# Kernel tuning notes

Measured on AMD Instinct MI355X. Metric: run time of the kernel, lower is better.

## Reference

```python
import jax, jax.numpy as jnp
import numpy as np

N = 20000      # nodes
E = 320000     # edges
D = 512        # width
L = 4          # layers
VOCAB = 256
MAX_POS = 256
EPS = 1e-5


def setup_inputs() -> dict:
    key = jax.random.key(0)
    ks = jax.random.split(key, 12)
    tokens = jax.random.randint(ks[0], (N,), 0, VOCAB)
    pos = jax.random.randint(ks[1], (N,), 0, MAX_POS)
    edge_index = jax.random.randint(ks[2], (2, E), 0, N)
    vocab_emb = jax.random.normal(ks[3], (VOCAB, D), jnp.float32) * 0.05
    pos_emb = jax.random.normal(ks[4], (MAX_POS, D), jnp.float32) * 0.05
    bn_gamma = jnp.ones((L, D), jnp.float32)
    bn_beta = jnp.zeros((L, D), jnp.float32)
    bn_mean = jax.random.normal(ks[5], (L, D), jnp.float32) * 0.1
    bn_var = jax.random.uniform(ks[6], (L, D), jnp.float32, 0.5, 1.5)
    W_rel = jax.random.normal(ks[7], (L, D, D), jnp.float32) * (1.0 / np.sqrt(D))
    b_rel = jnp.zeros((L, D), jnp.float32)
    W_root = jax.random.normal(ks[8], (L, D, D), jnp.float32) * (1.0 / np.sqrt(D))
    return {
        "tokens": tokens, "pos": pos, "edge_index": edge_index,
        "vocab_emb": vocab_emb, "pos_emb": pos_emb,
        "bn_gamma": bn_gamma, "bn_beta": bn_beta,
        "bn_mean": bn_mean, "bn_var": bn_var,
        "W_rel": W_rel, "b_rel": b_rel, "W_root": W_root,
    }


def reference(tokens, pos, edge_index, vocab_emb, pos_emb,
              bn_gamma, bn_beta, bn_mean, bn_var, W_rel, b_rel, W_root):
    src, dst = edge_index[0], edge_index[1]
    # in-degree for mean aggregation (clamped to 1 like PyG mean aggr)
    deg = jax.ops.segment_sum(jnp.ones((E,), jnp.float32), dst, num_segments=N)
    deg = jnp.maximum(deg, 1.0)[:, None]                     # [N,1]

    x = vocab_emb[tokens] + pos_emb[pos]                     # [N,D]
    for l in range(L):
        # BatchNorm1d, eval mode with running stats
        inv = bn_gamma[l] * jax.lax.rsqrt(bn_var[l] + EPS)
        x = (x - bn_mean[l]) * inv + bn_beta[l]
        # GraphConv: W_root x_i + W_rel * mean_{j->i} x_j + b
        agg = jax.ops.segment_sum(x[src], dst, num_segments=N) / deg
        x = agg @ W_rel[l].T + b_rel[l] + x @ W_root[l].T
        x = jax.nn.relu(x)
    return x
```

## Files before the change

kernel.cpp:

```cpp
#include <hip/hip_runtime.h>
#include <cstdint>

#define EPS 1e-5f

typedef __attribute__((ext_vector_type(8))) short bf16x8;
typedef __attribute__((ext_vector_type(4))) float f32x4;

__device__ __forceinline__ unsigned short f2bf(float x) {
    uint32_t u = __float_as_uint(x);
    u += 0x7fffu + ((u >> 16) & 1u);
    return (unsigned short)(u >> 16);
}
__device__ __forceinline__ uint32_t pack2(float lo, float hi) {
    return (uint32_t)f2bf(lo) | ((uint32_t)f2bf(hi) << 16);
}
__device__ __forceinline__ float bflo(uint32_t p) { return __uint_as_float(p << 16); }
__device__ __forceinline__ float bfhi(uint32_t p) { return __uint_as_float(p & 0xffff0000u); }

__device__ __forceinline__ void async_ld16(const void* g, const void* l) {
    __builtin_amdgcn_global_load_lds(
        (const __attribute__((address_space(1))) uint32_t*)(uintptr_t)g,
        (__attribute__((address_space(3))) uint32_t*)(uint32_t)(uintptr_t)l,
        16, 0, 0);
}

__global__ __launch_bounds__(256) void zero_kernel(int* __restrict__ p, int n) {
    int i = blockIdx.x * 256 + threadIdx.x;
    if (i < n) p[i] = 0;
}

__global__ __launch_bounds__(256) void count_kernel(const int* __restrict__ ei,
                                                    int* __restrict__ deg, int E) {
    int e = blockIdx.x * 256 + threadIdx.x;
    if (e < E) atomicAdd(&deg[ei[E + e]], 1);
}

__global__ __launch_bounds__(1024) void scan_kernel(const int* __restrict__ deg,
                                                    int* __restrict__ offsets,
                                                    int* __restrict__ cursor,
                                                    float* __restrict__ deginv, int N) {
    __shared__ int part[1024];
    const int t = threadIdx.x;
    const int CH = (N + 1023) >> 10;
    const int base = t * CH;
    int s = 0;
    for (int j = 0; j < CH; ++j) {
        int idx = base + j;
        if (idx < N) s += deg[idx];
    }
    part[t] = s;
    __syncthreads();
    for (int off = 1; off < 1024; off <<= 1) {
        int add = (t >= off) ? part[t - off] : 0;
        __syncthreads();
        part[t] += add;
        __syncthreads();
    }
    int run = (t == 0) ? 0 : part[t - 1];
    for (int j = 0; j < CH; ++j) {
        int idx = base + j;
        if (idx < N) {
            offsets[idx] = run;
            cursor[idx]  = run;
            int dgi = deg[idx];
            deginv[idx] = 1.0f / (float)(dgi > 0 ? dgi : 1);
            run += dgi;
        }
    }
    if (t == 1023) offsets[N] = run;
}

__global__ __launch_bounds__(256) void fill_kernel(const int* __restrict__ ei,
                                                   int* __restrict__ cursor,
                                                   int* __restrict__ csr, int E) {
    int e = blockIdx.x * 256 + threadIdx.x;
    if (e < E) {
        int dd = ei[E + e];
        int slot = atomicAdd(&cursor[dd], 1);
        csr[slot] = ei[e];
    }
}

__global__ __launch_bounds__(256) void embed_bn_kernel(const int* __restrict__ tok,
                                                       const int* __restrict__ pos,
                                                       const float* __restrict__ vemb,
                                                       const float* __restrict__ pemb,
                                                       const float* __restrict__ gamma,
                                                       const float* __restrict__ beta,
                                                       const float* __restrict__ mean,
                                                       const float* __restrict__ var,
                                                       uint32_t* __restrict__ Acat, int N) {
    const int idx = blockIdx.x * 256 + threadIdx.x;
    if (idx >= N * 128) return;
    const int row = idx >> 7;
    const int c = (idx & 127) * 4;
    const int tk = tok[row];
    const int ps = pos[row];
    const float4 a = *(const float4*)&vemb[(size_t)tk * 512 + c];
    const float4 b = *(const float4*)&pemb[(size_t)ps * 512 + c];
    const float4 g = *(const float4*)&gamma[c];
    const float4 be = *(const float4*)&beta[c];
    const float4 mn = *(const float4*)&mean[c];
    const float4 vr = *(const float4*)&var[c];
    const float y0 = (a.x + b.x - mn.x) * (g.x * rsqrtf(vr.x + EPS)) + be.x;
    const float y1 = (a.y + b.y - mn.y) * (g.y * rsqrtf(vr.y + EPS)) + be.y;
    const float y2 = (a.z + b.z - mn.z) * (g.z * rsqrtf(vr.z + EPS)) + be.z;
    const float y3 = (a.w + b.w - mn.w) * (g.w * rsqrtf(vr.w + EPS)) + be.w;
    uint2 o;
    o.x = pack2(y0, y1);
    o.y = pack2(y2, y3);
    *(uint2*)&Acat[(size_t)row * 512 + (c >> 1)] = o;
}

__global__ __launch_bounds__(256) void castW_kernel(const float* __restrict__ Wroot,
                                                    const float* __restrict__ Wrel,
                                                    uint32_t* __restrict__ Wcat) {
    const int p = blockIdx.x * 256 + threadIdx.x;
    const int o  = p >> 9;
    const int dp = p & 511;
    float2 v;
    if (dp < 256) v = *(const float2*)&Wroot[(size_t)o * 512 + dp * 2];
    else          v = *(const float2*)&Wrel[(size_t)o * 512 + (dp - 256) * 2];
    Wcat[(size_t)o * 512 + dp] = pack2(v.x, v.y);
}

__global__ __launch_bounds__(256) void aggregate_kernel(uint32_t* __restrict__ Acat,
                                                        const int* __restrict__ offsets,
                                                        const int* __restrict__ csr,
                                                        const float* __restrict__ deginv,
                                                        int N) {
    const int node = blockIdx.x * 4 + (threadIdx.x >> 6);
    if (node >= N) return;
    const int lane = threadIdx.x & 63;
    const int col = lane * 4;
    const int beg = offsets[node];
    const int end = offsets[node + 1];
    float s[8] = {0.f, 0.f, 0.f, 0.f, 0.f, 0.f, 0.f, 0.f};
    int e = beg;
    for (; e + 4 <= end; e += 4) {
        const int i0 = csr[e];
        const int i1 = csr[e + 1];
        const int i2 = csr[e + 2];
        const int i3 = csr[e + 3];
        const uint4 p0 = *(const uint4*)&Acat[(size_t)i0 * 512 + col];
        const uint4 p1 = *(const uint4*)&Acat[(size_t)i1 * 512 + col];
        const uint4 p2 = *(const uint4*)&Acat[(size_t)i2 * 512 + col];
        const uint4 p3 = *(const uint4*)&Acat[(size_t)i3 * 512 + col];
        s[0] += bflo(p0.x) + bflo(p1.x) + bflo(p2.x) + bflo(p3.x);
        s[1] += bfhi(p0.x) + bfhi(p1.x) + bfhi(p2.x) + bfhi(p3.x);
        s[2] += bflo(p0.y) + bflo(p1.y) + bflo(p2.y) + bflo(p3.y);
        s[3] += bfhi(p0.y) + bfhi(p1.y) + bfhi(p2.y) + bfhi(p3.y);
        s[4] += bflo(p0.z) + bflo(p1.z) + bflo(p2.z) + bflo(p3.z);
        s[5] += bfhi(p0.z) + bfhi(p1.z) + bfhi(p2.z) + bfhi(p3.z);
        s[6] += bflo(p0.w) + bflo(p1.w) + bflo(p2.w) + bflo(p3.w);
        s[7] += bfhi(p0.w) + bfhi(p1.w) + bfhi(p2.w) + bfhi(p3.w);
    }
    for (; e < end; ++e) {
        const int i0 = csr[e];
        const uint4 p0 = *(const uint4*)&Acat[(size_t)i0 * 512 + col];
        s[0] += bflo(p0.x); s[1] += bfhi(p0.x);
        s[2] += bflo(p0.y); s[3] += bfhi(p0.y);
        s[4] += bflo(p0.z); s[5] += bfhi(p0.z);
        s[6] += bflo(p0.w); s[7] += bfhi(p0.w);
    }
    const float inv = deginv[node];
    uint4 o;
    o.x = pack2(s[0] * inv, s[1] * inv);
    o.y = pack2(s[2] * inv, s[3] * inv);
    o.z = pack2(s[4] * inv, s[5] * inv);
    o.w = pack2(s[6] * inv, s[7] * inv);
    *(uint4*)&Acat[(size_t)node * 512 + 256 + col] = o;
}

__global__ __launch_bounds__(256) void gemm_bt_bias_relu(const unsigned short* __restrict__ A,
                                                         const unsigned short* __restrict__ B,
                                                         const float* __restrict__ bias,
                                                         const float* __restrict__ gamma,
                                                         const float* __restrict__ beta,
                                                         const float* __restrict__ mean,
                                                         const float* __restrict__ var,
                                                         int last,
                                                         float* __restrict__ C,
                                                         unsigned short* __restrict__ Abn,
                                                         int M) {
    __shared__ __align__(16) unsigned short As[128 * 32];
    __shared__ __align__(16) unsigned short Bs[128 * 32];

    const int t    = threadIdx.x;
    const int lane = t & 63;
    const int wave = t >> 6;
    const int wm = (wave >> 1) * 64;
    const int wn = (wave & 1) * 64;
    const int bm = blockIdx.y;
    const int bn = blockIdx.x;

    const int r  = t >> 2;
    const int kc = t & 3;
    int ar0 = bm * 128 + r;      if (ar0 >= M) ar0 = M - 1;
    int ar1 = bm * 128 + r + 64; if (ar1 >= M) ar1 = M - 1;
    const int br0 = bn * 128 + r;
    const int br1 = br0 + 64;

    const unsigned short* ga0 = A + (size_t)ar0 * 1024 + kc * 8;
    const unsigned short* ga1 = A + (size_t)ar1 * 1024 + kc * 8;
    const unsigned short* gb0 = B + (size_t)br0 * 1024 + kc * 8;
    const unsigned short* gb1 = B + (size_t)br1 * 1024 + kc * 8;

    unsigned short* la0 = &As[r * 32 + kc * 8];
    unsigned short* la1 = &As[(r + 64) * 32 + kc * 8];
    unsigned short* lb0 = &Bs[r * 32 + kc * 8];
    unsigned short* lb1 = &Bs[(r + 64) * 32 + kc * 8];

    const f32x4 zero = {0.f, 0.f, 0.f, 0.f};
    f32x4 acc[4][4];
#pragma unroll
    for (int i = 0; i < 4; ++i)
#pragma unroll
        for (int j = 0; j < 4; ++j) acc[i][j] = zero;

    const int lm = lane & 15;
    const int q  = lane >> 4;

    for (int k0 = 0; k0 < 1024; k0 += 32) {
        async_ld16(ga0 + k0, la0);
        async_ld16(ga1 + k0, la1);
        async_ld16(gb0 + k0, lb0);
        async_ld16(gb1 + k0, lb1);
        __syncthreads();

        bf16x8 afr[4], bfr[4];
#pragma unroll
        for (int mt = 0; mt < 4; ++mt)
            afr[mt] = *(const bf16x8*)&As[(wm + mt * 16 + lm) * 32 + q * 8];
#pragma unroll
        for (int nt = 0; nt < 4; ++nt)
            bfr[nt] = *(const bf16x8*)&Bs[(wn + nt * 16 + lm) * 32 + q * 8];
#pragma unroll
        for (int mt = 0; mt < 4; ++mt)
#pragma unroll
            for (int nt = 0; nt < 4; ++nt)
                acc[mt][nt] = __builtin_amdgcn_mfma_f32_16x16x32_bf16(afr[mt], bfr[nt],
                                                                     acc[mt][nt], 0, 0, 0);
        __syncthreads();
    }

#pragma unroll
    for (int nt = 0; nt < 4; ++nt) {
        const int col = bn * 128 + wn + nt * 16 + lm;
        const float bv = bias[col];
        float bn_inv = 0.f, bn_mb = 0.f;
        if (!last) {
            bn_inv = gamma[col] * rsqrtf(var[col] + EPS);
            bn_mb  = mean[col];
        }
        const float bn_beta = last ? 0.f : beta[col];
#pragma unroll
        for (int mt = 0; mt < 4; ++mt) {
            const int row0 = bm * 128 + wm + mt * 16 + q * 4;
#pragma unroll
            for (int i = 0; i < 4; ++i) {
                const int row = row0 + i;
                if (row < M) {
                    float v = acc[mt][nt][i] + bv;
                    v = v > 0.f ? v : 0.f;
                    if (last) {
                        C[(size_t)row * 512 + col] = v;
                    } else {
                        const float y = (v - bn_mb) * bn_inv + bn_beta;
                        Abn[(size_t)row * 1024 + col] = f2bf(y);
                    }
                }
            }
        }
    }
}

extern "C" void kernel_launch(void* const* d_in, const int* in_sizes, int n_in,
                              void* d_out, int out_size, void* d_ws, size_t ws_size,
                              hipStream_t stream) {
    const int*   tokens = (const int*)d_in[0];
    const int*   posi   = (const int*)d_in[1];
    const int*   ei     = (const int*)d_in[2];
    const float* vemb   = (const float*)d_in[3];
    const float* pemb   = (const float*)d_in[4];
    const float* gamma  = (const float*)d_in[5];
    const float* beta   = (const float*)d_in[6];
    const float* mean   = (const float*)d_in[7];
    const float* var    = (const float*)d_in[8];
    const float* Wrel   = (const float*)d_in[9];
    const float* brel   = (const float*)d_in[10];
    const float* Wroot  = (const float*)d_in[11];

    const int N = in_sizes[0];
    const int E = in_sizes[2] / 2;
    float* out = (float*)d_out;

    char* w = (char*)d_ws;
    int*      deg     = (int*)(w);
    int*      offsets = (int*)(w + 80000);
    int*      cursor  = (int*)(w + 160016);
    float*    deginv  = (float*)(w + 240032);
    int*      csr     = (int*)(w + 320048);
    uint32_t* Acat    = (uint32_t*)(w + 1600064);
    uint32_t* Wcat    = (uint32_t*)(w + 42560064);

    zero_kernel<<<(N + 255) / 256, 256, 0, stream>>>(deg, N);
    count_kernel<<<(E + 255) / 256, 256, 0, stream>>>(ei, deg, E);
    scan_kernel<<<1, 1024, 0, stream>>>(deg, offsets, cursor, deginv, N);
    fill_kernel<<<(E + 255) / 256, 256, 0, stream>>>(ei, cursor, csr, E);

    embed_bn_kernel<<<(N * 128 + 255) / 256, 256, 0, stream>>>(
        tokens, posi, vemb, pemb, gamma, beta, mean, var, Acat, N);

    for (int l = 0; l < 4; ++l) {
        const int last = (l == 3);
        castW_kernel<<<1024, 256, 0, stream>>>(Wroot + (size_t)l * 262144,
                                               Wrel + (size_t)l * 262144, Wcat);
        aggregate_kernel<<<(N + 3) / 4, 256, 0, stream>>>(Acat, offsets, csr, deginv, N);
        gemm_bt_bias_relu<<<dim3(4, (N + 127) / 128), 256, 0, stream>>>(
            (const unsigned short*)Acat, (const unsigned short*)Wcat, brel + l * 512,
            gamma + (l + 1) * 512, beta + (l + 1) * 512,
            mean + (l + 1) * 512, var + (l + 1) * 512,
            last, out, (unsigned short*)Acat, N);
    }
}
```

Baseline: 563.4 us.

## Replace GEMM with triple-buffered 256x128 tile kernel using swizzled LDS and XCD mapping

Replaces the single-buffered 128x128 GEMM with a 512-thread, 256x128-tile kernel. It uses a three-stage async global-to-LDS pipeline over K=64 slices with explicit vmcnt waits, XOR-swizzled LDS layout to avoid bank conflicts, and s_setprio around MFMA bursts. Block IDs are remapped so each XCD works on a contiguous band of row tiles, which is meant to improve L2 reuse of A. It uses 144 KB of dynamic LDS per block, which limits occupancy, and it relies on hand-counted waitcnt values.

```diff
diff --git a/kernel.cpp b/kernel.cpp
--- a/kernel.cpp
+++ b/kernel.cpp
@@ -172,44 +172,65 @@
     *(uint4*)&Acat[(size_t)node * 512 + 256 + col] = o;
 }
 
-__global__ __launch_bounds__(256) void gemm_bt_bias_relu(const unsigned short* __restrict__ A,
-                                                         const unsigned short* __restrict__ B,
-                                                         const float* __restrict__ bias,
-                                                         const float* __restrict__ gamma,
-                                                         const float* __restrict__ beta,
-                                                         const float* __restrict__ mean,
-                                                         const float* __restrict__ var,
-                                                         int last,
-                                                         float* __restrict__ C,
-                                                         unsigned short* __restrict__ Abn,
-                                                         int M) {
-    __shared__ __align__(16) unsigned short As[128 * 32];
-    __shared__ __align__(16) unsigned short Bs[128 * 32];
+__global__ __launch_bounds__(512, 2)
+void gemm_pipe(const unsigned short* __restrict__ A,
+               const unsigned short* __restrict__ B,
+               const float* __restrict__ bias,
+               const float* __restrict__ gamma,
+               const float* __restrict__ beta,
+               const float* __restrict__ mean,
+               const float* __restrict__ var,
+               int last,
+               float* __restrict__ C,
+               unsigned short* __restrict__ Abn,
+               int M, int mt, int rpx) {
+    extern __shared__ unsigned short lds[];
+
+    const int bid = blockIdx.x;
+    const int xcd = bid & 7;
+    const int slt = bid >> 3;
+    const int bm  = xcd * rpx + (slt >> 2);
+    const int bn  = slt & 3;
+    if (bm >= mt) return;
 
     const int t    = threadIdx.x;
     const int lane = t & 63;
-    const int wave = t >> 6;
-    const int wm = (wave >> 1) * 64;
-    const int wn = (wave & 1) * 64;
-    const int bm = blockIdx.y;
-    const int bn = blockIdx.x;
-
-    const int r  = t >> 2;
-    const int kc = t & 3;
-    int ar0 = bm * 128 + r;      if (ar0 >= M) ar0 = M - 1;
-    int ar1 = bm * 128 + r + 64; if (ar1 >= M) ar1 = M - 1;
-    const int br0 = bn * 128 + r;
-    const int br1 = br0 + 64;
-
-    const unsigned short* ga0 = A + (size_t)ar0 * 1024 + kc * 8;
-    const unsigned short* ga1 = A + (size_t)ar1 * 1024 + kc * 8;
-    const unsigned short* gb0 = B + (size_t)br0 * 1024 + kc * 8;
-    const unsigned short* gb1 = B + (size_t)br1 * 1024 + kc * 8;
-
-    unsigned short* la0 = &As[r * 32 + kc * 8];
-    unsigned short* la1 = &As[(r + 64) * 32 + kc * 8];
-    unsigned short* lb0 = &Bs[r * 32 + kc * 8];
-    unsigned short* lb1 = &Bs[(r + 64) * 32 + kc * 8];
+    const int wid  = t >> 6;
+    const int wr   = wid >> 1;
+    const int wc   = wid & 1;
+    const int lm   = lane & 15;
+    const int q    = lane >> 4;
+
+    const int tr = t >> 3;
+    const int sg = (t & 7) ^ (tr & 7);
+    int r0 = bm * 256 + tr;        if (r0 >= M) r0 = M - 1;
+    int r1 = bm * 256 + 64  + tr;  if (r1 >= M) r1 = M - 1;
+    int r2 = bm * 256 + 128 + tr;  if (r2 >= M) r2 = M - 1;
+    int r3 = bm * 256 + 192 + tr;  if (r3 >= M) r3 = M - 1;
+    const unsigned short* gA0 = A + (size_t)r0 * 1024 + sg * 8;
+    const unsigned short* gA1 = A + (size_t)r1 * 1024 + sg * 8;
+    const unsigned short* gA2 = A + (size_t)r2 * 1024 + sg * 8;
+    const unsigned short* gA3 = A + (size_t)r3 * 1024 + sg * 8;
+    const unsigned short* gB0 = B + (size_t)(bn * 128 + tr)      * 1024 + sg * 8;
+    const unsigned short* gB1 = B + (size_t)(bn * 128 + 64 + tr) * 1024 + sg * 8;
+    const int ldst = t * 8;
+
+#define STAGE_H0(KT, LP) do {                                          \
+        async_ld16(gA0 + (KT) * 64, (LP) + 0 * 4096 + ldst);           \
+        async_ld16(gA1 + (KT) * 64, (LP) + 1 * 4096 + ldst);           \
+        async_ld16(gA2 + (KT) * 64, (LP) + 2 * 4096 + ldst);           \
+    } while (0)
+#define STAGE_H1(KT, LP) do {                                          \
+        async_ld16(gA3 + (KT) * 64, (LP) + 3 * 4096 + ldst);           \
+        async_ld16(gB0 + (KT) * 64, (LP) + 16384 + 0 * 4096 + ldst);   \
+        async_ld16(gB1 + (KT) * 64, (LP) + 16384 + 1 * 4096 + ldst);   \
+    } while (0)
+
+    const int aB = (wr * 64 + lm) * 64;
+    const int bB = 16384 + (wc * 64 + lm) * 64;
+    const int sw = lm & 7;
+    const int k0 = ((0 + q) ^ sw) * 8;
+    const int k1 = ((4 + q) ^ sw) * 8;
 
     const f32x4 zero = {0.f, 0.f, 0.f, 0.f};
     f32x4 acc[4][4];
@@ -218,61 +239,74 @@
 #pragma unroll
         for (int j = 0; j < 4; ++j) acc[i][j] = zero;
 
-    const int lm = lane & 15;
-    const int q  = lane >> 4;
-
-    for (int k0 = 0; k0 < 1024; k0 += 32) {
-        async_ld16(ga0 + k0, la0);
-        async_ld16(ga1 + k0, la1);
-        async_ld16(gb0 + k0, lb0);
-        async_ld16(gb1 + k0, lb1);
-        __syncthreads();
-
-        bf16x8 afr[4], bfr[4];
-#pragma unroll
-        for (int mt = 0; mt < 4; ++mt)
-            afr[mt] = *(const bf16x8*)&As[(wm + mt * 16 + lm) * 32 + q * 8];
-#pragma unroll
-        for (int nt = 0; nt < 4; ++nt)
-            bfr[nt] = *(const bf16x8*)&Bs[(wn + nt * 16 + lm) * 32 + q * 8];
-#pragma unroll
-        for (int mt = 0; mt < 4; ++mt)
-#pragma unroll
-            for (int nt = 0; nt < 4; ++nt)
-                acc[mt][nt] = __builtin_amdgcn_mfma_f32_16x16x32_bf16(afr[mt], bfr[nt],
-                                                                     acc[mt][nt], 0, 0, 0);
-        __syncthreads();
-    }
-
-#pragma unroll
-    for (int nt = 0; nt < 4; ++nt) {
-        const int col = bn * 128 + wn + nt * 16 + lm;
-        const float bv = bias[col];
-        float bn_inv = 0.f, bn_mb = 0.f;
+#define MFMA_PHASE(KOFF) do {                                                   \
+        bf16x8 afr[4], bfr[4];                                                  \
+        _Pragma("unroll") for (int mf = 0; mf < 4; ++mf)                        \
+            afr[mf] = *(const bf16x8*)&Lb[aB + mf * 1024 + (KOFF)];             \
+        _Pragma("unroll") for (int nf = 0; nf < 4; ++nf)                        \
+            bfr[nf] = *(const bf16x8*)&Lb[bB + nf * 1024 + (KOFF)];             \
+        __builtin_amdgcn_s_setprio(1);                                          \
+        _Pragma("unroll") for (int mf = 0; mf < 4; ++mf)                        \
+            _Pragma("unroll") for (int nf = 0; nf < 4; ++nf)                    \
+                acc[mf][nf] = __builtin_amdgcn_mfma_f32_16x16x32_bf16(          \
+                    afr[mf], bfr[nf], acc[mf][nf], 0, 0, 0);                    \
+        __builtin_amdgcn_s_setprio(0);                                          \
+    } while (0)
+
+    {
+        unsigned short* L0 = lds;
+        STAGE_H0(0, L0); STAGE_H1(0, L0);
+        unsigned short* L1 = lds + 24576;
+        STAGE_H0(1, L1); STAGE_H1(1, L1);
+    }
+
+#pragma unroll
+    for (int kt = 0; kt < 16; ++kt) {
+        unsigned short* Lb = lds + (kt % 3) * 24576;
+        unsigned short* Ln = lds + ((kt + 2) % 3) * 24576;
+        if (kt < 15) asm volatile("s_waitcnt vmcnt(6)" ::: "memory");
+        else         asm volatile("s_waitcnt vmcnt(0)" ::: "memory");
+        __builtin_amdgcn_s_barrier();
+        __builtin_amdgcn_sched_barrier(0);
+
+        if (kt + 2 < 16) STAGE_H0(kt + 2, Ln);
+        MFMA_PHASE(k0);
+        if (kt + 2 < 16) STAGE_H1(kt + 2, Ln);
+        MFMA_PHASE(k1);
+    }
+
+#pragma unroll
+    for (int nf = 0; nf < 4; ++nf) {
+        const int col = bn * 128 + wc * 64 + nf * 16 + lm;
+        const float bsv = bias[col];
+        float bn_inv = 0.f, bn_mb = 0.f, bn_bt = 0.f;
         if (!last) {
             bn_inv = gamma[col] * rsqrtf(var[col] + EPS);
             bn_mb  = mean[col];
+            bn_bt  = beta[col];
         }
-        const float bn_beta = last ? 0.f : beta[col];
-#pragma unroll
-        for (int mt = 0; mt < 4; ++mt) {
-            const int row0 = bm * 128 + wm + mt * 16 + q * 4;
+#pragma unroll
+        for (int mf = 0; mf < 4; ++mf) {
+            const int row0 = bm * 256 + wr * 64 + mf * 16 + q * 4;
 #pragma unroll
             for (int i = 0; i < 4; ++i) {
                 const int row = row0 + i;
                 if (row < M) {
-                    float v = acc[mt][nt][i] + bv;
+                    float v = acc[mf][nf][i] + bsv;
                     v = v > 0.f ? v : 0.f;
                     if (last) {
                         C[(size_t)row * 512 + col] = v;
                     } else {
-                        const float y = (v - bn_mb) * bn_inv + bn_beta;
+                        const float y = (v - bn_mb) * bn_inv + bn_bt;
                         Abn[(size_t)row * 1024 + col] = f2bf(y);
                     }
                 }
             }
         }
     }
+#undef STAGE_H0
+#undef STAGE_H1
+#undef MFMA_PHASE
 }
 
 extern "C" void kernel_launch(void* const* d_in, const int* in_sizes, int n_in,
@@ -304,6 +338,13 @@
     uint32_t* Acat    = (uint32_t*)(w + 1600064);
     uint32_t* Wcat    = (uint32_t*)(w + 42560064);
 
+    static bool s_attr = false;
+    if (!s_attr) {
+        (void)hipFuncSetAttribute(reinterpret_cast<const void*>(gemm_pipe),
+                                  hipFuncAttributeMaxDynamicSharedMemorySize, 147456);
+        s_attr = true;
+    }
+
     zero_kernel<<<(N + 255) / 256, 256, 0, stream>>>(deg, N);
     count_kernel<<<(E + 255) / 256, 256, 0, stream>>>(ei, deg, E);
     scan_kernel<<<1, 1024, 0, stream>>>(deg, offsets, cursor, deginv, N);
@@ -311,16 +352,20 @@
 
     embed_bn_kernel<<<(N * 128 + 255) / 256, 256, 0, stream>>>(
         tokens, posi, vemb, pemb, gamma, beta, mean, var, Acat, N);
+
+    const int mt  = (N + 255) >> 8;
+    const int rpx = (mt + 7) >> 3;
+    const int gb  = 8 * rpx * 4;
 
     for (int l = 0; l < 4; ++l) {
         const int last = (l == 3);
         castW_kernel<<<1024, 256, 0, stream>>>(Wroot + (size_t)l * 262144,
                                                Wrel + (size_t)l * 262144, Wcat);
         aggregate_kernel<<<(N + 3) / 4, 256, 0, stream>>>(Acat, offsets, csr, deginv, N);
-        gemm_bt_bias_relu<<<dim3(4, (N + 127) / 128), 256, 0, stream>>>(
+        gemm_pipe<<<gb, 512, 147456, stream>>>(
             (const unsigned short*)Acat, (const unsigned short*)Wcat, brel + l * 512,
             gamma + (l + 1) * 512, beta + (l + 1) * 512,
             mean + (l + 1) * 512, var + (l + 1) * 512,
-            last, out, (unsigned short*)Acat, N);
-    }
-}
+            last, out, (unsigned short*)Acat, N, mt, rpx);
+    }
+}
```

Result: slower. 597.1 us (+6.0%).

## Widen GEMM K-step to 64, swizzle block order, batch weight casts

Applied to the files above, without the earlier changes.

The GEMM now loads two 32-wide K slices per iteration, which halves the number of barrier pairs and issues more MFMAs between syncs. Blocks move to a 1D grid whose index is remapped so that consecutive blocks are spread across eight row groups, with the four column tiles of a row block kept adjacent, to change cache/XCD locality. When the workspace is large enough, all four layers' weights are cast to bf16 in one kernel up front instead of once per layer. This doubles LDS use per block and relies on a workspace-size check to choose the path.

```diff
diff --git a/kernel.cpp b/kernel.cpp
--- a/kernel.cpp
+++ b/kernel.cpp
@@ -122,6 +122,20 @@
     if (dp < 256) v = *(const float2*)&Wroot[(size_t)o * 512 + dp * 2];
     else          v = *(const float2*)&Wrel[(size_t)o * 512 + (dp - 256) * 2];
     Wcat[(size_t)o * 512 + dp] = pack2(v.x, v.y);
+}
+
+__global__ __launch_bounds__(256) void castW4_kernel(const float* __restrict__ Wroot,
+                                                     const float* __restrict__ Wrel,
+                                                     uint32_t* __restrict__ Wcat4) {
+    const int p = blockIdx.x * 256 + threadIdx.x;
+    const int l   = p >> 18;
+    const int rem = p & 262143;
+    const int o   = rem >> 9;
+    const int dp  = rem & 511;
+    float2 v;
+    if (dp < 256) v = *(const float2*)&Wroot[(size_t)l * 262144 + (size_t)o * 512 + dp * 2];
+    else          v = *(const float2*)&Wrel[(size_t)l * 262144 + (size_t)o * 512 + (dp - 256) * 2];
+    Wcat4[(size_t)l * 262144 + (size_t)o * 512 + dp] = pack2(v.x, v.y);
 }
 
 __global__ __launch_bounds__(256) void aggregate_kernel(uint32_t* __restrict__ Acat,
@@ -182,17 +196,20 @@
                                                          int last,
                                                          float* __restrict__ C,
                                                          unsigned short* __restrict__ Abn,
-                                                         int M) {
-    __shared__ __align__(16) unsigned short As[128 * 32];
-    __shared__ __align__(16) unsigned short Bs[128 * 32];
+                                                         int M, int mt, int rpx) {
+    __shared__ __align__(16) unsigned short As[2 * 128 * 32];
+    __shared__ __align__(16) unsigned short Bs[2 * 128 * 32];
+
+    const int bid = blockIdx.x;
+    const int bm  = (bid & 7) * rpx + ((bid >> 3) >> 2);
+    const int bn  = (bid >> 3) & 3;
+    if (bm >= mt) return;
 
     const int t    = threadIdx.x;
     const int lane = t & 63;
     const int wave = t >> 6;
     const int wm = (wave >> 1) * 64;
     const int wn = (wave & 1) * 64;
-    const int bm = blockIdx.y;
-    const int bn = blockIdx.x;
 
     const int r  = t >> 2;
     const int kc = t & 3;
@@ -206,10 +223,14 @@
     const unsigned short* gb0 = B + (size_t)br0 * 1024 + kc * 8;
     const unsigned short* gb1 = B + (size_t)br1 * 1024 + kc * 8;
 
-    unsigned short* la0 = &As[r * 32 + kc * 8];
-    unsigned short* la1 = &As[(r + 64) * 32 + kc * 8];
-    unsigned short* lb0 = &Bs[r * 32 + kc * 8];
-    unsigned short* lb1 = &Bs[(r + 64) * 32 + kc * 8];
+    unsigned short* la00 = &As[r * 32 + kc * 8];
+    unsigned short* la10 = &As[(r + 64) * 32 + kc * 8];
+    unsigned short* la01 = &As[4096 + r * 32 + kc * 8];
+    unsigned short* la11 = &As[4096 + (r + 64) * 32 + kc * 8];
+    unsigned short* lb00 = &Bs[r * 32 + kc * 8];
+    unsigned short* lb10 = &Bs[(r + 64) * 32 + kc * 8];
+    unsigned short* lb01 = &Bs[4096 + r * 32 + kc * 8];
+    unsigned short* lb11 = &Bs[4096 + (r + 64) * 32 + kc * 8];
 
     const f32x4 zero = {0.f, 0.f, 0.f, 0.f};
     f32x4 acc[4][4];
@@ -221,26 +242,35 @@
     const int lm = lane & 15;
     const int q  = lane >> 4;
 
-    for (int k0 = 0; k0 < 1024; k0 += 32) {
-        async_ld16(ga0 + k0, la0);
-        async_ld16(ga1 + k0, la1);
-        async_ld16(gb0 + k0, lb0);
-        async_ld16(gb1 + k0, lb1);
+    for (int k0 = 0; k0 < 1024; k0 += 64) {
+        async_ld16(ga0 + k0,      la00);
+        async_ld16(ga0 + k0 + 32, la01);
+        async_ld16(ga1 + k0,      la10);
+        async_ld16(ga1 + k0 + 32, la11);
+        async_ld16(gb0 + k0,      lb00);
+        async_ld16(gb0 + k0 + 32, lb01);
+        async_ld16(gb1 + k0,      lb10);
+        async_ld16(gb1 + k0 + 32, lb11);
         __syncthreads();
 
-        bf16x8 afr[4], bfr[4];
-#pragma unroll
-        for (int mt = 0; mt < 4; ++mt)
-            afr[mt] = *(const bf16x8*)&As[(wm + mt * 16 + lm) * 32 + q * 8];
-#pragma unroll
-        for (int nt = 0; nt < 4; ++nt)
-            bfr[nt] = *(const bf16x8*)&Bs[(wn + nt * 16 + lm) * 32 + q * 8];
-#pragma unroll
-        for (int mt = 0; mt < 4; ++mt)
+        bf16x8 afr[4][2], bfr[4][2];
+#pragma unroll
+        for (int kk = 0; kk < 2; ++kk) {
+#pragma unroll
+            for (int mt2 = 0; mt2 < 4; ++mt2)
+                afr[mt2][kk] = *(const bf16x8*)&As[kk * 4096 + (wm + mt2 * 16 + lm) * 32 + q * 8];
 #pragma unroll
             for (int nt = 0; nt < 4; ++nt)
-                acc[mt][nt] = __builtin_amdgcn_mfma_f32_16x16x32_bf16(afr[mt], bfr[nt],
-                                                                     acc[mt][nt], 0, 0, 0);
+                bfr[nt][kk] = *(const bf16x8*)&Bs[kk * 4096 + (wn + nt * 16 + lm) * 32 + q * 8];
+        }
+#pragma unroll
+        for (int kk = 0; kk < 2; ++kk)
+#pragma unroll
+            for (int mt2 = 0; mt2 < 4; ++mt2)
+#pragma unroll
+                for (int nt = 0; nt < 4; ++nt)
+                    acc[mt2][nt] = __builtin_amdgcn_mfma_f32_16x16x32_bf16(
+                        afr[mt2][kk], bfr[nt][kk], acc[mt2][nt], 0, 0, 0);
         __syncthreads();
     }
 
@@ -255,13 +285,13 @@
         }
         const float bn_beta = last ? 0.f : beta[col];
 #pragma unroll
-        for (int mt = 0; mt < 4; ++mt) {
-            const int row0 = bm * 128 + wm + mt * 16 + q * 4;
+        for (int mt2 = 0; mt2 < 4; ++mt2) {
+            const int row0 = bm * 128 + wm + mt2 * 16 + q * 4;
 #pragma unroll
             for (int i = 0; i < 4; ++i) {
                 const int row = row0 + i;
                 if (row < M) {
-                    float v = acc[mt][nt][i] + bv;
+                    float v = acc[mt2][nt][i] + bv;
                     v = v > 0.f ? v : 0.f;
                     if (last) {
                         C[(size_t)row * 512 + col] = v;
@@ -304,6 +334,8 @@
     uint32_t* Acat    = (uint32_t*)(w + 1600064);
     uint32_t* Wcat    = (uint32_t*)(w + 42560064);
 
+    const int batched = (ws_size >= 46754368ull) ? 1 : 0;
+
     zero_kernel<<<(N + 255) / 256, 256, 0, stream>>>(deg, N);
     count_kernel<<<(E + 255) / 256, 256, 0, stream>>>(ei, deg, E);
     scan_kernel<<<1, 1024, 0, stream>>>(deg, offsets, cursor, deginv, N);
@@ -312,15 +344,24 @@
     embed_bn_kernel<<<(N * 128 + 255) / 256, 256, 0, stream>>>(
         tokens, posi, vemb, pemb, gamma, beta, mean, var, Acat, N);
 
+    if (batched)
+        castW4_kernel<<<4096, 256, 0, stream>>>(Wroot, Wrel, Wcat);
+
+    const int mt  = (N + 127) >> 7;
+    const int rpx = (mt + 7) >> 3;
+    const int gb  = 8 * rpx * 4;
+
     for (int l = 0; l < 4; ++l) {
         const int last = (l == 3);
-        castW_kernel<<<1024, 256, 0, stream>>>(Wroot + (size_t)l * 262144,
-                                               Wrel + (size_t)l * 262144, Wcat);
+        if (!batched)
+            castW_kernel<<<1024, 256, 0, stream>>>(Wroot + (size_t)l * 262144,
+                                                   Wrel + (size_t)l * 262144, Wcat);
         aggregate_kernel<<<(N + 3) / 4, 256, 0, stream>>>(Acat, offsets, csr, deginv, N);
-        gemm_bt_bias_relu<<<dim3(4, (N + 127) / 128), 256, 0, stream>>>(
-            (const unsigned short*)Acat, (const unsigned short*)Wcat, brel + l * 512,
+        const uint32_t* Wl = batched ? (Wcat + (size_t)l * 262144) : Wcat;
+        gemm_bt_bias_relu<<<gb, 256, 0, stream>>>(
+            (const unsigned short*)Acat, (const unsigned short*)Wl, brel + l * 512,
             gamma + (l + 1) * 512, beta + (l + 1) * 512,
             mean + (l + 1) * 512, var + (l + 1) * 512,
-            last, out, (unsigned short*)Acat, N);
-    }
-}
+            last, out, (unsigned short*)Acat, N, mt, rpx);
+    }
+}
```

After: 626.0 us. 1.11x slower.
